# Optimization experiments

Measured on AMD Instinct MI355X. Metric: run time of the kernel, lower is better.

The kernel has to match this reference:

```python
import jax, jax.numpy as jnp
import numpy as np

FP4_CODE = np.array([-6, -4, -3, -2, -1.5, -1, -0.5, -0.0,
                     0.0, 0.5, 1, 1.5, 2, 3, 4, 6], dtype=np.float32)


def setup_inputs() -> dict:
    key = jax.random.key(0)
    k1, k2 = jax.random.split(key)
    rows, cols = 4096, 4096
    x = jax.random.normal(k1, (rows, cols), dtype=jnp.float32)
    # per-row positive scale, as produced by find_params (abs-max / (maxq/2)); keep away from 0
    scale = jax.random.uniform(k2, (rows, 1), dtype=jnp.float32, minval=0.1, maxval=1.0)
    code = jnp.asarray(FP4_CODE)  # 16-entry fp4 codebook from configure(bits=4)
    return {"x": x, "scale": scale, "code": code}


def reference(x, scale, code):
    # q = x / scale; nearest codeword by absolute distance; dequantize by scale
    q = x / scale                                   # [R, C]
    dist = jnp.abs(q[..., None] - code)             # [R, C, 16] broadcasted distance
    idx = jnp.argmin(dist, axis=-1)                 # [R, C] (first min on ties, like torch)
    xq = code[idx] * scale                          # gather + rescale
    return xq
```

## Files before the change

### kernel.cpp

```cpp
#include <hip/hip_runtime.h>


__global__ __launch_bounds__(256) void fp4_quant_kernel(
    const float* __restrict__ x,
    const float* __restrict__ scale,
    const float* __restrict__ code,
    float* __restrict__ out,
    int n4,
    int row_shift)
{
    int gid = blockIdx.x * blockDim.x + threadIdx.x;
    if (gid >= n4) return;

    float c[16];
#pragma unroll
    for (int j = 0; j < 16; ++j) c[j] = code[j];

    const int row = gid >> row_shift;
    const float s = scale[row];

    const float4 xv = reinterpret_cast<const float4*>(x)[gid];
    float q[4] = { xv.x / s, xv.y / s, xv.z / s, xv.w / s };
    float r[4];

#pragma unroll
    for (int e = 0; e < 4; ++e) {
        float best = fabsf(q[e] - c[0]);
        float val  = c[0];
#pragma unroll
        for (int j = 1; j < 16; ++j) {
            float d  = fabsf(q[e] - c[j]);
            bool lt  = d < best;
            best = lt ? d : best;
            val  = lt ? c[j] : val;
        }
        r[e] = val * s;
    }

    float4 ov;
    ov.x = r[0]; ov.y = r[1]; ov.z = r[2]; ov.w = r[3];
    reinterpret_cast<float4*>(out)[gid] = ov;
}

extern "C" void kernel_launch(void* const* d_in, const int* in_sizes, int n_in,
                              void* d_out, int out_size, void* d_ws, size_t ws_size,
                              hipStream_t stream) {
    const float* x     = (const float*)d_in[0];
    const float* scale = (const float*)d_in[1];
    const float* code  = (const float*)d_in[2];
    float* out         = (float*)d_out;

    const int n    = in_sizes[0];
    const int rows = in_sizes[1];
    const int cols = n / rows;
    const int cols4 = cols / 4;

    int row_shift = 0;
    while ((1 << row_shift) < cols4) ++row_shift;

    const int n4 = n / 4;
    const int block = 256;
    const int grid = (n4 + block - 1) / block;
    fp4_quant_kernel<<<grid, block, 0, stream>>>(x, scale, code, out, n4, row_shift);
}
```

Baseline: 123.2 us.

## Replace argmin search with sorted-codebook count, reciprocal divide, two float4 per thread

The codebook is now staged in shared memory with the duplicate -0.0 entry dropped, giving 15 sorted entries. Each element finds its nearest codeword by counting how often the distance decreases along that sorted list, then reads the result through a shared-memory lookup, which replaces the compare-and-select argmin chain. Division is replaced by a reciprocal multiply plus an FMA correction step that aims to reproduce the exact quotient. Each thread now handles two float4 chunks of the same row, halving the thread count. The counting trick relies on the codebook being sorted and on its tie behaviour matching first-min argmin, and the shared lookup indexed by a per-lane value may cause bank conflicts.

```diff
diff --git a/kernel.cpp b/kernel.cpp
--- a/kernel.cpp
+++ b/kernel.cpp
@@ -6,40 +6,60 @@
     const float* __restrict__ scale,
     const float* __restrict__ code,
     float* __restrict__ out,
-    int n4,
-    int row_shift)
+    int n8,
+    int row_shift,
+    int col_mask,
+    int cols4)
 {
-    int gid = blockIdx.x * blockDim.x + threadIdx.x;
-    if (gid >= n4) return;
+    __shared__ float cc[15];
+    if (threadIdx.x < 15) {
+        const int j = threadIdx.x;
+        cc[j] = code[j + (j >= 8 ? 1 : 0)];
+    }
+    __syncthreads();
 
-    float c[16];
+    const int tid = blockIdx.x * blockDim.x + threadIdx.x;
+    if (tid >= n8) return;
+
+    const int row  = tid >> row_shift;
+    const int col4 = tid & col_mask;
+    const long base = (long)row * cols4 + col4;
+    const int half_stride = col_mask + 1;
+
+    const float s = scale[row];
+    const float r = 1.0f / s;
+
+    float c[15];
 #pragma unroll
-    for (int j = 0; j < 16; ++j) c[j] = code[j];
+    for (int j = 0; j < 15; ++j) c[j] = cc[j];
 
-    const int row = gid >> row_shift;
-    const float s = scale[row];
-
-    const float4 xv = reinterpret_cast<const float4*>(x)[gid];
-    float q[4] = { xv.x / s, xv.y / s, xv.z / s, xv.w / s };
-    float r[4];
+    const float4* __restrict__ x4 = reinterpret_cast<const float4*>(x);
+    float4* __restrict__ o4 = reinterpret_cast<float4*>(out);
 
 #pragma unroll
-    for (int e = 0; e < 4; ++e) {
-        float best = fabsf(q[e] - c[0]);
-        float val  = c[0];
+    for (int half = 0; half < 2; ++half) {
+        const long idx = base + (long)half * half_stride;
+        const float4 xv = x4[idx];
+        float xe[4] = { xv.x, xv.y, xv.z, xv.w };
+        float re[4];
 #pragma unroll
-        for (int j = 1; j < 16; ++j) {
-            float d  = fabsf(q[e] - c[j]);
-            bool lt  = d < best;
-            best = lt ? d : best;
-            val  = lt ? c[j] : val;
+        for (int e = 0; e < 4; ++e) {
+            const float a  = xe[e];
+            const float q0 = a * r;
+            const float q  = fmaf(r, fmaf(-s, q0, a), q0);
+            int cnt = 0;
+            float prev = fabsf(q - c[0]);
+#pragma unroll
+            for (int j = 1; j < 15; ++j) {
+                const float cur = fabsf(q - c[j]);
+                cnt += (cur < prev) ? 1 : 0;
+                prev = cur;
+            }
+            re[e] = cc[cnt] * s;
         }
-        r[e] = val * s;
+        float4 ov = { re[0], re[1], re[2], re[3] };
+        o4[idx] = ov;
     }
-
-    float4 ov;
-    ov.x = r[0]; ov.y = r[1]; ov.z = r[2]; ov.w = r[3];
-    reinterpret_cast<float4*>(out)[gid] = ov;
 }
 
 extern "C" void kernel_launch(void* const* d_in, const int* in_sizes, int n_in,
@@ -54,12 +74,15 @@
     const int rows = in_sizes[1];
     const int cols = n / rows;
     const int cols4 = cols / 4;
+    const int tpr  = cols / 8;
 
     int row_shift = 0;
-    while ((1 << row_shift) < cols4) ++row_shift;
+    while ((1 << row_shift) < tpr) ++row_shift;
+    const int col_mask = tpr - 1;
 
-    const int n4 = n / 4;
+    const int n8 = n / 8;
     const int block = 256;
-    const int grid = (n4 + block - 1) / block;
-    fp4_quant_kernel<<<grid, block, 0, stream>>>(x, scale, code, out, n4, row_shift);
+    const int grid = (n8 + block - 1) / block;
+    fp4_quant_kernel<<<grid, block, 0, stream>>>(x, scale, code, out,
+                                                 n8, row_shift, col_mask, cols4);
 }
```

Result: no change. 121.3 us (-1.6%).
